# Optimization experiments

Hardware: AMD Instinct MI355X
Metric: run time of the kernel (lower is better)

## Reference

```python
import jax, jax.numpy as jnp
import numpy as np

B, H, W = 128, 32, 32
INF = 1e9
EPS = 1e-6  # strictly positive weights -> dist strictly decreases along backtrack (no tie cycles)
OFFS = np.array([(-1, -1), (-1, 0), (-1, 1), (0, -1), (0, 1), (1, -1), (1, 0), (1, 1)], dtype=np.int32)


def _neighbor_min(d):
    # d: [B,H,W] -> per-cell min over 8-neighborhood (INF outside the grid)
    p = jnp.pad(d, ((0, 0), (1, 1), (1, 1)), constant_values=INF)
    sh = jnp.stack([p[:, 1 + dr:1 + dr + H, 1 + dc:1 + dc + W] for dr, dc in OFFS], axis=0)
    return jnp.min(sh, axis=0)


def solve(weights, source, target):
    """Dijkstra/A*(h=0)-equivalent shortest path on an 8-connected grid.
    Entering cell v costs weights[v]; returns a [B,H,W] 0/1 mask of the optimal path
    (source and target cells included). Computed exactly via Bellman-Ford relaxation
    (H*W sweeps >= max hop count) followed by greedy min-dist backtracking.
    """
    w = weights + EPS
    b = jnp.arange(B)
    sr, sc = source[:, 0], source[:, 1]
    ws = w[b, sr, sc]
    dist0 = jnp.full((B, H, W), INF, w.dtype).at[b, sr, sc].set(ws)

    def bf_step(dist, _):
        return jnp.minimum(dist, w + _neighbor_min(dist)), None

    dist, _ = jax.lax.scan(bf_step, dist0, None, length=H * W)

    dist_flat = dist.reshape(B, H * W)
    offs = jnp.asarray(OFFS)  # [8,2]
    hw = jnp.array([H, W], offs.dtype)

    def bt_step(carry, _):
        pos, mask, done = carry            # pos [B,2], mask [B,H,W], done [B]
        r, c = pos[:, 0], pos[:, 1]
        mask = mask.at[b, r, c].max((~done).astype(mask.dtype))
        done = done | ((r == sr) & (c == sc))
        cand = pos[:, None, :] + offs[None]               # [B,8,2]
        valid = ((cand >= 0) & (cand < hw)).all(-1)       # [B,8]
        cr = jnp.clip(cand[..., 0], 0, H - 1)
        cc = jnp.clip(cand[..., 1], 0, W - 1)
        dvals = jnp.take_along_axis(dist_flat, cr * W + cc, axis=1)
        dvals = jnp.where(valid, dvals, INF)
        j = jnp.argmin(dvals, axis=1)                     # predecessor = min-dist neighbor
        nxt = jnp.stack([cr[b, j], cc[b, j]], axis=1)
        pos = jnp.where(done[:, None], pos, nxt)
        return (pos, mask, done), None

    mask0 = jnp.zeros((B, H, W), weights.dtype)
    done0 = jnp.zeros((B,), bool)
    (_, paths, _), _ = jax.lax.scan(bt_step, (target.astype(offs.dtype), mask0, done0), None, length=H * W)
    return paths


def setup_inputs() -> dict:
    key = jax.random.key(0)
    k1, k2, k3 = jax.random.split(key, 3)
    return {
        "weights": jax.random.uniform(k1, (B, H, W), jnp.float32),
        "source": jax.random.randint(k2, (B, 2), 0, H),
        "target": jax.random.randint(k3, (B, 2), 0, H),
    }


def reference(weights, source, target):
    # BBAStar.forward: paths come straight from a_star_batch (the autograd.Function
    # forward is identity on paths); exp_nodes is solver-internal bookkeeping and is
    # not part of the math being differentiated, so we return the path masks.
    return solve(weights, source, target)
```

## Files before the change

### kernel.cpp

```cpp
#include <hip/hip_runtime.h>

#define GH 32
#define GW 32
#define PITCH 34
#define NPAD (PITCH * PITCH)
#define INFV 1000000000.0f
#define EPSV 1e-6f

__global__ __launch_bounds__(1024)
void bbastar_kernel(const float* __restrict__ weights,
                    const int* __restrict__ source,
                    const int* __restrict__ target,
                    float* __restrict__ out) {
    __shared__ float d[NPAD];
    __shared__ int flags[16];

    const int b   = blockIdx.x;
    const int tid = threadIdx.x;
    const int r   = tid >> 5;
    const int c   = tid & 31;
    const int addr = (r + 1) * PITCH + (c + 1);

    const int sr = source[2 * b];
    const int sc = source[2 * b + 1];

    const float w = weights[b * (GH * GW) + tid] + EPSV;

    out[b * (GH * GW) + tid] = 0.0f;

    for (int i = tid; i < NPAD; i += 1024) d[i] = INFV;
    __syncthreads();
    const bool is_src = (r == sr) && (c == sc);
    float myd = is_src ? w : INFV;
    if (is_src) d[addr] = w;
    __syncthreads();

    for (int it = 0; it < 2048; ++it) {
        const float n0 = d[addr - PITCH - 1];
        const float n1 = d[addr - PITCH];
        const float n2 = d[addr - PITCH + 1];
        const float n3 = d[addr - 1];
        const float n4 = d[addr + 1];
        const float n5 = d[addr + PITCH - 1];
        const float n6 = d[addr + PITCH];
        const float n7 = d[addr + PITCH + 1];
        const float nmin = fminf(fminf(fminf(n0, n1), fminf(n2, n3)),
                                 fminf(fminf(n4, n5), fminf(n6, n7)));
        const float nd = w + nmin;
        const bool ch = nd < myd;
        if (ch) { myd = nd; d[addr] = nd; }

        const unsigned long long bal = __ballot(ch);
        if ((tid & 63) == 0) flags[tid >> 6] = (bal != 0ULL) ? 1 : 0;
        __syncthreads();
        int any = 0;
        #pragma unroll
        for (int i = 0; i < 16; ++i) any |= flags[i];
        if (!any) break;
        __syncthreads();
    }

    if (tid == 0) {
        const int drr[8] = {-1, -1, -1,  0, 0,  1, 1, 1};
        const int dcc[8] = {-1,  0,  1, -1, 1, -1, 0, 1};
        int pr = target[2 * b];
        int pc = target[2 * b + 1];
        float* ob = out + b * (GH * GW);
        for (int step = 0; step < GH * GW; ++step) {
            ob[pr * GW + pc] = 1.0f;
            if (pr == sr && pc == sc) break;
            float best = INFV;
            int bj = 0;
            #pragma unroll
            for (int j = 0; j < 8; ++j) {
                const float v = d[(pr + drr[j] + 1) * PITCH + (pc + dcc[j] + 1)];
                if (v < best) { best = v; bj = j; }
            }
            pr += drr[bj];
            pc += dcc[bj];
        }
    }
}

extern "C" void kernel_launch(void* const* d_in, const int* in_sizes, int n_in,
                              void* d_out, int out_size, void* d_ws, size_t ws_size,
                              hipStream_t stream) {
    const float* weights = (const float*)d_in[0];
    const int*   source  = (const int*)d_in[1];
    const int*   target  = (const int*)d_in[2];
    float*       out     = (float*)d_out;
    const int B = in_sizes[0] / (GH * GW);
    bbastar_kernel<<<B, 1024, 0, stream>>>(weights, source, target, out);
}
```

Baseline: 84.13 us.

## Process four cells per thread with alternating in-row sweeps and one barrier

Each thread now owns four consecutive cells in a row, so the block drops from 1024 to 256 threads and loads and stores use float4. Neighbour values in the shared top and bottom rows are reused across the four cells, and in-row neighbours come from registers with a sweep direction that alternates each iteration, so a relaxation can travel further per iteration (Gauss-Seidel style). The convergence flags are double-buffered, which removes the second __syncthreads per iteration. The cost is more serial work per thread and fewer waves per block; mixing register and shared values may also change the order in which updates become visible.

```diff
diff --git a/kernel.cpp b/kernel.cpp
--- a/kernel.cpp
+++ b/kernel.cpp
@@ -7,57 +7,79 @@
 #define INFV 1000000000.0f
 #define EPSV 1e-6f
 
-__global__ __launch_bounds__(1024)
+__global__ __launch_bounds__(256)
 void bbastar_kernel(const float* __restrict__ weights,
                     const int* __restrict__ source,
                     const int* __restrict__ target,
                     float* __restrict__ out) {
     __shared__ float d[NPAD];
-    __shared__ int flags[16];
+    __shared__ int flags[2][4];
 
     const int b   = blockIdx.x;
     const int tid = threadIdx.x;
-    const int r   = tid >> 5;
-    const int c   = tid & 31;
-    const int addr = (r + 1) * PITCH + (c + 1);
+    const int r   = tid >> 3;
+    const int q   = tid & 7;
+    const int c0  = q << 2;
+    const int base = (r + 1) * PITCH + (c0 + 1);
 
     const int sr = source[2 * b];
     const int sc = source[2 * b + 1];
 
-    const float w = weights[b * (GH * GW) + tid] + EPSV;
+    const float4 w4 = ((const float4*)(weights + b * (GH * GW)))[tid];
+    float w[4] = { w4.x + EPSV, w4.y + EPSV, w4.z + EPSV, w4.w + EPSV };
 
-    out[b * (GH * GW) + tid] = 0.0f;
+    ((float4*)(out + b * (GH * GW)))[tid] = make_float4(0.f, 0.f, 0.f, 0.f);
 
-    for (int i = tid; i < NPAD; i += 1024) d[i] = INFV;
+    for (int i = tid; i < NPAD; i += 256) d[i] = INFV;
     __syncthreads();
-    const bool is_src = (r == sr) && (c == sc);
-    float myd = is_src ? w : INFV;
-    if (is_src) d[addr] = w;
+    float myd[4];
+    #pragma unroll
+    for (int k = 0; k < 4; ++k) {
+        const bool is_src = (r == sr) && (c0 + k == sc);
+        myd[k] = is_src ? w[k] : INFV;
+        if (is_src) d[base + k] = w[k];
+    }
     __syncthreads();
 
     for (int it = 0; it < 2048; ++it) {
-        const float n0 = d[addr - PITCH - 1];
-        const float n1 = d[addr - PITCH];
-        const float n2 = d[addr - PITCH + 1];
-        const float n3 = d[addr - 1];
-        const float n4 = d[addr + 1];
-        const float n5 = d[addr + PITCH - 1];
-        const float n6 = d[addr + PITCH];
-        const float n7 = d[addr + PITCH + 1];
-        const float nmin = fminf(fminf(fminf(n0, n1), fminf(n2, n3)),
-                                 fminf(fminf(n4, n5), fminf(n6, n7)));
-        const float nd = w + nmin;
-        const bool ch = nd < myd;
-        if (ch) { myd = nd; d[addr] = nd; }
+        float t[6], btm[6];
+        #pragma unroll
+        for (int k = 0; k < 6; ++k) {
+            t[k]   = d[base - PITCH - 1 + k];
+            btm[k] = d[base + PITCH - 1 + k];
+        }
+        const float lft = d[base - 1];
+        const float rgt = d[base + 4];
+
+        bool ch = false;
+        if ((it & 1) == 0) {
+            #pragma unroll
+            for (int k = 0; k < 4; ++k) {
+                const float lnb = (k == 0) ? lft : myd[k - 1];
+                const float rnb = (k == 3) ? rgt : myd[k + 1];
+                const float nmin = fminf(fminf(fminf(t[k], t[k + 1]), fminf(t[k + 2], btm[k])),
+                                         fminf(fminf(btm[k + 1], btm[k + 2]), fminf(lnb, rnb)));
+                const float nd = w[k] + nmin;
+                if (nd < myd[k]) { myd[k] = nd; d[base + k] = nd; ch = true; }
+            }
+        } else {
+            #pragma unroll
+            for (int k = 3; k >= 0; --k) {
+                const float lnb = (k == 0) ? lft : myd[k - 1];
+                const float rnb = (k == 3) ? rgt : myd[k + 1];
+                const float nmin = fminf(fminf(fminf(t[k], t[k + 1]), fminf(t[k + 2], btm[k])),
+                                         fminf(fminf(btm[k + 1], btm[k + 2]), fminf(lnb, rnb)));
+                const float nd = w[k] + nmin;
+                if (nd < myd[k]) { myd[k] = nd; d[base + k] = nd; ch = true; }
+            }
+        }
 
         const unsigned long long bal = __ballot(ch);
-        if ((tid & 63) == 0) flags[tid >> 6] = (bal != 0ULL) ? 1 : 0;
+        if ((tid & 63) == 0) flags[it & 1][tid >> 6] = (bal != 0ULL) ? 1 : 0;
         __syncthreads();
-        int any = 0;
-        #pragma unroll
-        for (int i = 0; i < 16; ++i) any |= flags[i];
+        const int any = flags[it & 1][0] | flags[it & 1][1] |
+                        flags[it & 1][2] | flags[it & 1][3];
         if (!any) break;
-        __syncthreads();
     }
 
     if (tid == 0) {
@@ -90,5 +112,5 @@
     const int*   target  = (const int*)d_in[2];
     float*       out     = (float*)d_out;
     const int B = in_sizes[0] / (GH * GW);
-    bbastar_kernel<<<B, 1024, 0, stream>>>(weights, source, target, out);
+    bbastar_kernel<<<B, 256, 0, stream>>>(weights, source, target, out);
 }
```

Result: faster. 79.94 us (-5.0%).

## Process two grids per wavefront with row-per-lane sweeps and alternating directions

Applied to the files above, without the earlier changes.

Replaces the 1024-thread-per-grid Jacobi relaxation with one 64-lane wavefront that handles two grids, each lane owning a full row in registers. Each sweep runs a Gauss-Seidel pass along the row, alternating left-to-right and right-to-left, so values travel far in one step and fewer iterations are needed. Only one wavefront now has to synchronise, which removes the cross-wave flag reduction. The trade-offs are serial per-lane work of 32 cells per sweep and a hard cap of 1200 iterations, which could stop early on adversarial grids.

```diff
diff --git a/kernel.cpp b/kernel.cpp
--- a/kernel.cpp
+++ b/kernel.cpp
@@ -2,78 +2,144 @@
 
 #define GH 32
 #define GW 32
-#define PITCH 34
-#define NPAD (PITCH * PITCH)
+#define PITCH 36
+#define DNP (34 * PITCH + 4)
+#define WNP (GH * PITCH)
 #define INFV 1000000000.0f
 #define EPSV 1e-6f
 
-__global__ __launch_bounds__(1024)
+
+__global__ __launch_bounds__(64)
 void bbastar_kernel(const float* __restrict__ weights,
                     const int* __restrict__ source,
                     const int* __restrict__ target,
                     float* __restrict__ out) {
-    __shared__ float d[NPAD];
-    __shared__ int flags[16];
+    __shared__ float d[2][DNP];
+    __shared__ float wl[2][WNP];
 
-    const int b   = blockIdx.x;
-    const int tid = threadIdx.x;
-    const int r   = tid >> 5;
-    const int c   = tid & 31;
-    const int addr = (r + 1) * PITCH + (c + 1);
+    const int lane = threadIdx.x;
+    const int sb   = lane >> 5;
+    const int r    = lane & 31;
+    const int gb   = blockIdx.x * 2 + sb;
 
-    const int sr = source[2 * b];
-    const int sc = source[2 * b + 1];
+    {
+        const float4* wg = (const float4*)(weights + (size_t)blockIdx.x * 2048);
+        #pragma unroll
+        for (int i = 0; i < 8; ++i) {
+            const int idx = lane + i * 64;
+            float4 v = wg[idx];
+            const int fi = idx << 2;
+            const int bb = fi >> 10;
+            const int rr = (fi >> 5) & 31;
+            const int cc = fi & 31;
+            *(float4*)&wl[bb][rr * PITCH + 4 + cc] =
+                make_float4(v.x + EPSV, v.y + EPSV, v.z + EPSV, v.w + EPSV);
+        }
+    }
+    {
+        const float4 inf4 = make_float4(INFV, INFV, INFV, INFV);
+        float4* df4 = (float4*)&d[0][0];
+        #pragma unroll
+        for (int i = 0; i < 10; ++i) {
+            const int idx = lane + i * 64;
+            if (idx < 614) df4[idx] = inf4;
+        }
+    }
+    {
+        const float4 z = make_float4(0.f, 0.f, 0.f, 0.f);
+        float4* og = (float4*)(out + (size_t)blockIdx.x * 2048);
+        #pragma unroll
+        for (int i = 0; i < 8; ++i) og[lane + i * 64] = z;
+    }
 
-    const float w = weights[b * (GH * GW) + tid] + EPSV;
-
-    out[b * (GH * GW) + tid] = 0.0f;
-
-    for (int i = tid; i < NPAD; i += 1024) d[i] = INFV;
+    const int sr = source[2 * gb], sc = source[2 * gb + 1];
     __syncthreads();
-    const bool is_src = (r == sr) && (c == sc);
-    float myd = is_src ? w : INFV;
-    if (is_src) d[addr] = w;
+    if (r == 0)
+        d[sb][(sr + 1) * PITCH + 4 + sc] = wl[sb][sr * PITCH + 4 + sc];
     __syncthreads();
 
-    for (int it = 0; it < 2048; ++it) {
-        const float n0 = d[addr - PITCH - 1];
-        const float n1 = d[addr - PITCH];
-        const float n2 = d[addr - PITCH + 1];
-        const float n3 = d[addr - 1];
-        const float n4 = d[addr + 1];
-        const float n5 = d[addr + PITCH - 1];
-        const float n6 = d[addr + PITCH];
-        const float n7 = d[addr + PITCH + 1];
-        const float nmin = fminf(fminf(fminf(n0, n1), fminf(n2, n3)),
-                                 fminf(fminf(n4, n5), fminf(n6, n7)));
-        const float nd = w + nmin;
-        const bool ch = nd < myd;
-        if (ch) { myd = nd; d[addr] = nd; }
+    float w[32], own[32];
+    {
+        const float4* wr = (const float4*)&wl[sb][r * PITCH + 4];
+        const float4* dr = (const float4*)&d[sb][(r + 1) * PITCH + 4];
+        #pragma unroll
+        for (int k = 0; k < 8; ++k) {
+            const float4 v = wr[k];
+            w[4*k] = v.x; w[4*k+1] = v.y; w[4*k+2] = v.z; w[4*k+3] = v.w;
+            const float4 o = dr[k];
+            own[4*k] = o.x; own[4*k+1] = o.y; own[4*k+2] = o.z; own[4*k+3] = o.w;
+        }
+    }
+    float* db = d[sb];
+    const int topb = r * PITCH + 3;
+    const int botb = (r + 2) * PITCH + 3;
+    const int ownb = (r + 1) * PITCH + 4;
 
-        const unsigned long long bal = __ballot(ch);
-        if ((tid & 63) == 0) flags[tid >> 6] = (bal != 0ULL) ? 1 : 0;
+    for (int it = 0; it < 1200; ++it) {
+        float top[34], bot[34];
+        top[0] = db[topb];  bot[0] = db[botb];
+        #pragma unroll
+        for (int k = 0; k < 8; ++k) {
+            const float4 t = *(const float4*)&db[topb + 1 + 4*k];
+            top[1+4*k] = t.x; top[2+4*k] = t.y; top[3+4*k] = t.z; top[4+4*k] = t.w;
+            const float4 bo = *(const float4*)&db[botb + 1 + 4*k];
+            bot[1+4*k] = bo.x; bot[2+4*k] = bo.y; bot[3+4*k] = bo.z; bot[4+4*k] = bo.w;
+        }
+        top[33] = db[topb + 33];  bot[33] = db[botb + 33];
+
+        float mx = 0.0f;
+        if ((it & 1) == 0) {
+            float left = INFV;
+            #pragma unroll
+            for (int c = 0; c < 32; ++c) {
+                const float oldr = (c < 31) ? own[c+1] : INFV;
+                const float m1 = fminf(fminf(top[c], top[c+1]), top[c+2]);
+                const float m2 = fminf(fminf(bot[c], bot[c+1]), bot[c+2]);
+                const float m  = fminf(fminf(m1, m2), oldr);
+                const float a  = fminf(own[c], w[c] + m);
+                const float nd = fminf(a, w[c] + left);
+                mx   = fmaxf(mx, own[c] - nd);
+                own[c] = nd;
+                left = nd;
+            }
+        } else {
+            float right = INFV;
+            #pragma unroll
+            for (int c = 31; c >= 0; --c) {
+                const float oldl = (c > 0) ? own[c-1] : INFV;
+                const float m1 = fminf(fminf(top[c], top[c+1]), top[c+2]);
+                const float m2 = fminf(fminf(bot[c], bot[c+1]), bot[c+2]);
+                const float m  = fminf(fminf(m1, m2), oldl);
+                const float a  = fminf(own[c], w[c] + m);
+                const float nd = fminf(a, w[c] + right);
+                mx    = fmaxf(mx, own[c] - nd);
+                own[c] = nd;
+                right = nd;
+            }
+        }
+        #pragma unroll
+        for (int k = 0; k < 8; ++k)
+            *(float4*)&db[ownb + 4*k] =
+                make_float4(own[4*k], own[4*k+1], own[4*k+2], own[4*k+3]);
+
+        const unsigned long long bal = __ballot(mx > 0.0f);
         __syncthreads();
-        int any = 0;
-        #pragma unroll
-        for (int i = 0; i < 16; ++i) any |= flags[i];
-        if (!any) break;
-        __syncthreads();
+        if (bal == 0ULL) break;
     }
 
-    if (tid == 0) {
+    if (r == 0) {
         const int drr[8] = {-1, -1, -1,  0, 0,  1, 1, 1};
         const int dcc[8] = {-1,  0,  1, -1, 1, -1, 0, 1};
-        int pr = target[2 * b];
-        int pc = target[2 * b + 1];
-        float* ob = out + b * (GH * GW);
+        int pr = target[2 * gb];
+        int pc = target[2 * gb + 1];
+        float* ob = out + (size_t)gb * 1024;
         for (int step = 0; step < GH * GW; ++step) {
             ob[pr * GW + pc] = 1.0f;
             if (pr == sr && pc == sc) break;
-            float best = INFV;
-            int bj = 0;
+            float best = INFV; int bj = 0;
             #pragma unroll
             for (int j = 0; j < 8; ++j) {
-                const float v = d[(pr + drr[j] + 1) * PITCH + (pc + dcc[j] + 1)];
+                const float v = db[(pr + drr[j] + 1) * PITCH + 4 + (pc + dcc[j])];
                 if (v < best) { best = v; bj = j; }
             }
             pr += drr[bj];
@@ -90,5 +156,5 @@
     const int*   target  = (const int*)d_in[2];
     float*       out     = (float*)d_out;
     const int B = in_sizes[0] / (GH * GW);
-    bbastar_kernel<<<B, 1024, 0, stream>>>(weights, source, target, out);
+    bbastar_kernel<<<B / 2, 64, 0, stream>>>(weights, source, target, out);
 }
```

Measured after the change: 99.00 us. +17.7%, slower.
